# Performance work log

Hardware: AMD Instinct MI355X
Metric: run time of the kernel (lower is better)

Reference implementation:

```python
import jax, jax.numpy as jnp
import numpy as np

N, D, H, L, T, R = 50000, 128, 8, 2, 4, 8
E = 800000
HD = D // H  # head_size = 16
SQRT_D = float(np.sqrt(HD))


def typed_linear(x, types, W):
    # x: (n, Din), types: (n,), W: (T, Din, Dout)  -- per-type dense projection
    out = jnp.zeros((x.shape[0], W.shape[-1]), x.dtype)
    for t in range(W.shape[0]):
        out = out + jnp.where((types == t)[:, None], x @ W[t], 0.0)
    return out


def rel_typed(x, etype, W):
    # x: (E, H, d), etype: (E,), W: (H, R, d, d) -- per-head, per-edge-type linear
    out = jnp.zeros_like(x)
    for r in range(W.shape[1]):
        out = out + jnp.where((etype == r)[:, None, None], jnp.einsum('ehd,hdo->eho', x, W[:, r]), 0.0)
    return out


def edge_softmax(a, dst, n):
    # softmax over incoming edges per destination node, per head. a: (E, H)
    amax = jax.ops.segment_max(a, dst, num_segments=n)
    amax = jnp.where(jnp.isfinite(amax), amax, 0.0)
    ex = jnp.exp(a - amax[dst])
    s = jax.ops.segment_sum(ex, dst, num_segments=n)
    return ex / (s[dst] + 1e-9)


def layer_norm(x, g, b, eps=1e-5):
    mu = x.mean(-1, keepdims=True)
    var = ((x - mu) ** 2).mean(-1, keepdims=True)
    return (x - mu) * jax.lax.rsqrt(var + eps) * g + b


def hgt_conv(x, ntype, etype, src, dst, Wk, Wq, Wv, Wa, ratt, rmsg, rpri, skip):
    n = x.shape[0]
    k = typed_linear(x, ntype, Wk).reshape(n, H, HD)
    q = typed_linear(x, ntype, Wq).reshape(n, H, HD)
    v = typed_linear(x, ntype, Wv).reshape(n, H, HD)
    kw = rel_typed(k[src], etype, ratt)               # (E, H, d)
    pri = rpri[:, etype].T                            # (E, H)
    a = (kw * q[dst]).sum(-1) * pri / SQRT_D          # (E, H)
    m = rel_typed(v[src], etype, rmsg)                # (E, H, d)
    att = edge_softmax(a, dst, n)                     # (E, H)
    h = jax.ops.segment_sum(m * att[..., None], dst, num_segments=n)
    h = h.reshape(n, D)
    h = typed_linear(h, ntype, Wa)                    # dropout off (eval)
    alpha = jax.nn.sigmoid(skip[ntype])[:, None]
    return h * alpha + x * (1.0 - alpha)


def setup_inputs() -> dict:
    key = jax.random.key(0)
    ks = jax.random.split(key, 12)
    g_lin = float(np.sqrt(2.0 / (D + D)))   # xavier-ish scale for D x D
    g_rel = float(np.sqrt(2.0 / (HD + HD)))
    g_emb = float(np.sqrt(2.0 / (N + D)))
    return {
        'embed': jax.random.normal(ks[0], (T, N, D), jnp.float32) * g_emb,
        'Wk': jax.random.normal(ks[1], (L, T, D, D), jnp.float32) * g_lin,
        'Wq': jax.random.normal(ks[2], (L, T, D, D), jnp.float32) * g_lin,
        'Wv': jax.random.normal(ks[3], (L, T, D, D), jnp.float32) * g_lin,
        'Wa': jax.random.normal(ks[4], (L, T, D, D), jnp.float32) * g_lin,
        'rel_att': jax.random.normal(ks[5], (L, H, R, HD, HD), jnp.float32) * g_rel,
        'rel_msg': jax.random.normal(ks[6], (L, H, R, HD, HD), jnp.float32) * g_rel,
        'rel_pri': jnp.ones((L, H, R), jnp.float32),
        'skip': jnp.ones((L, T), jnp.float32),
        'ln_g': jnp.ones((L, D), jnp.float32),
        'ln_b': jnp.zeros((L, D), jnp.float32),
        'src': jax.random.randint(ks[7], (E,), 0, N, jnp.int32),
        'dst': jax.random.randint(ks[8], (E,), 0, N, jnp.int32),
        'ntype': jax.random.randint(ks[9], (N,), 0, T, jnp.int32),
        'etype': jax.random.randint(ks[10], (E,), 0, R, jnp.int32),
    }


def reference(embed, Wk, Wq, Wv, Wa, rel_att, rel_msg, rel_pri, skip, ln_g, ln_b, src, dst, ntype, etype):
    # masked per-type embedding init: node gets row <rank-within-its-type> of its type table
    onehot = jax.nn.one_hot(ntype, T, dtype=jnp.int32)
    rank = jnp.take_along_axis(jnp.cumsum(onehot, axis=0), ntype[:, None], axis=1)[:, 0] - 1
    h = embed[ntype, rank]                            # (N, D)
    for l in range(L):
        h_prev = h
        hc = hgt_conv(h, ntype, etype, src, dst,
                      Wk[l], Wq[l], Wv[l], Wa[l],
                      rel_att[l], rel_msg[l], rel_pri[l], skip[l])
        h = layer_norm(hc, ln_g[l], ln_b[l]) + h_prev
    return h
```

## Files before the change

kernel.cpp:

```cpp
#include <hip/hip_runtime.h>
#include <math.h>

#define N_NODES 50000
#define DIM     128
#define NHEAD   8
#define HDIM    16
#define NLAYER  2
#define NTYPE   4
#define NREL    8
#define NEDGE   800000
#define RB      256
#define GN      8
#define MT      32
#define NK      (N_NODES * NREL)

typedef __attribute__((ext_vector_type(8))) short bf16x8;
typedef __attribute__((ext_vector_type(4))) float f32x4;

__device__ __forceinline__ float blo(unsigned w) { return __uint_as_float(w << 16); }
__device__ __forceinline__ float bhi(unsigned w) { return __uint_as_float(w & 0xFFFF0000u); }
__device__ __forceinline__ unsigned short f2bf(float f) {
    unsigned b = __float_as_uint(f);
    b += 0x7FFFu + ((b >> 16) & 1u);
    return (unsigned short)(b >> 16);
}
__device__ __forceinline__ bf16x8 pack8(float4 x0, float4 x1) {
    bf16x8 r;
    r[0] = (short)f2bf(x0.x); r[1] = (short)f2bf(x0.y);
    r[2] = (short)f2bf(x0.z); r[3] = (short)f2bf(x0.w);
    r[4] = (short)f2bf(x1.x); r[5] = (short)f2bf(x1.y);
    r[6] = (short)f2bf(x1.z); r[7] = (short)f2bf(x1.w);
    return r;
}


__global__ void k_hist(const int* __restrict__ ntype, int* __restrict__ hist, int n) {
    __shared__ int cnt[NTYPE];
    if (threadIdx.x < NTYPE) cnt[threadIdx.x] = 0;
    __syncthreads();
    int i = blockIdx.x * RB + threadIdx.x;
    if (i < n) atomicAdd(&cnt[ntype[i]], 1);
    __syncthreads();
    if (threadIdx.x < NTYPE) hist[blockIdx.x * NTYPE + threadIdx.x] = cnt[threadIdx.x];
}

__global__ void k_prefix(const int* __restrict__ hist, int* __restrict__ off, int nb) {
    int t = threadIdx.x;
    if (t >= NTYPE) return;
    int acc = 0;
    for (int b = 0; b < nb; b++) { off[b * NTYPE + t] = acc; acc += hist[b * NTYPE + t]; }
}

__global__ void k_rank(const int* __restrict__ ntype, const int* __restrict__ off,
                       int* __restrict__ rank, int n) {
    __shared__ int ty[RB];
    int i = blockIdx.x * RB + threadIdx.x;
    int t = (i < n) ? ntype[i] : -1;
    ty[threadIdx.x] = t;
    __syncthreads();
    if (i < n) {
        int c = 0;
        for (int j = 0; j < (int)threadIdx.x; j++) c += (ty[j] == t);
        rank[i] = off[blockIdx.x * NTYPE + t] + c;
    }
}

__global__ void k_embed(const float* __restrict__ embed, const int* __restrict__ ntype,
                        const int* __restrict__ rank, float* __restrict__ h) {
    int i = blockIdx.x;
    int t = ntype[i], r = rank[i];
    h[(size_t)i * DIM + threadIdx.x] = embed[((size_t)t * N_NODES + r) * DIM + threadIdx.x];
}

__global__ void k_typeoff(const int* __restrict__ hist, const int* __restrict__ boff,
                          int nb, int* __restrict__ typeoff) {
    if (threadIdx.x == 0 && blockIdx.x == 0) {
        int acc = 0;
        for (int t = 0; t < NTYPE; t++) {
            typeoff[t] = acc;
            acc += boff[(nb - 1) * NTYPE + t] + hist[(nb - 1) * NTYPE + t];
        }
    }
}

__global__ void k_perm(const int* __restrict__ ntype, const int* __restrict__ rank,
                       const int* __restrict__ typeoff, int* __restrict__ perm, int n) {
    int i = blockIdx.x * 256 + threadIdx.x;
    if (i < n) perm[typeoff[ntype[i]] + rank[i]] = i;
}


__global__ void k_deg2(const int* __restrict__ dst, const int* __restrict__ etype,
                       int* __restrict__ deg) {
    int e = blockIdx.x * 256 + threadIdx.x;
    if (e < NEDGE) atomicAdd(&deg[dst[e] * NREL + etype[e]], 1);
}

__global__ void k_scan1(const int* __restrict__ deg, int* __restrict__ rs,
                        int* __restrict__ bsum, int n) {
    __shared__ int sh[256];
    int i = blockIdx.x * 256 + threadIdx.x;
    int v = (i < n) ? deg[i] : 0;
    sh[threadIdx.x] = v;
    __syncthreads();
    for (int off = 1; off < 256; off <<= 1) {
        int x = (threadIdx.x >= off) ? sh[threadIdx.x - off] : 0;
        __syncthreads();
        sh[threadIdx.x] += x;
        __syncthreads();
    }
    if (i < n) rs[i] = sh[threadIdx.x] - v;
    if (threadIdx.x == 255) bsum[blockIdx.x] = sh[255];
}

__global__ void k_scan2b(int* __restrict__ bsum, int nb) {
    __shared__ int sh[256];
    __shared__ int carry;
    if (threadIdx.x == 0) carry = 0;
    __syncthreads();
    for (int base = 0; base < nb; base += 256) {
        int i = base + threadIdx.x;
        int v = (i < nb) ? bsum[i] : 0;
        sh[threadIdx.x] = v;
        __syncthreads();
        for (int off = 1; off < 256; off <<= 1) {
            int x = (threadIdx.x >= off) ? sh[threadIdx.x - off] : 0;
            __syncthreads();
            sh[threadIdx.x] += x;
            __syncthreads();
        }
        if (i < nb) bsum[i] = sh[threadIdx.x] - v + carry;
        __syncthreads();
        if (threadIdx.x == 0) carry += sh[255];
        __syncthreads();
    }
}

__global__ void k_scan3(int* __restrict__ rs, const int* __restrict__ bsum, int n) {
    int i = blockIdx.x * 256 + threadIdx.x;
    if (i < n) rs[i] += bsum[blockIdx.x];
    if (i == 0) rs[n] = NEDGE;
}

__global__ void k_scatter2(const int* __restrict__ src, const int* __restrict__ dst,
                           const int* __restrict__ etype, const int* __restrict__ rs,
                           int* __restrict__ cur, int* __restrict__ epk) {
    int e = blockIdx.x * 256 + threadIdx.x;
    if (e < NEDGE) {
        int et = etype[e];
        int key = dst[e] * NREL + et;
        int p = atomicAdd(&cur[key], 1);
        epk[rs[key] + p] = src[e] | (et << 24);
    }
}


__global__ void k_rmsgT(const float* __restrict__ rmsg, float* __restrict__ rmsgT) {
    int b = blockIdx.x;
    int d = threadIdx.x >> 4, o = threadIdx.x & 15;
    rmsgT[b * 256 + o * 16 + d] = rmsg[b * 256 + d * 16 + o];
}

__global__ void k_rattB(const float* __restrict__ ratt, unsigned short* __restrict__ rattB) {
    int i = blockIdx.x * 256 + threadIdx.x;
    rattB[i] = f2bf(ratt[i]);
}

__global__ void k_packW(const float* __restrict__ W, unsigned short* __restrict__ WB) {
    int t = blockIdx.x;
    const float* w = W + (size_t)t * 16384;
    unsigned short* ob = WB + (size_t)t * 16384;
    for (int idx = threadIdx.x; idx < 16384; idx += 256) {
        int ct = idx >> 11, kc = (idx >> 9) & 3, l = (idx >> 3) & 63, j = idx & 7;
        int k = kc * 32 + ((l >> 4) << 3) + j;
        int c = ct * 16 + (l & 15);
        ob[idx] = f2bf(w[k * 128 + c]);
    }
}


__global__ __launch_bounds__(256) void k_qkv_mfma(
        const float* __restrict__ h, const int* __restrict__ perm, const int* __restrict__ ntype,
        const float* __restrict__ Wk, const float* __restrict__ Wq, const float* __restrict__ Wv,
        const unsigned short* __restrict__ WkB, const unsigned short* __restrict__ WqB,
        const unsigned short* __restrict__ WvB, const float* __restrict__ rmsgT,
        unsigned short* __restrict__ kb, float* __restrict__ qout,
        unsigned short* __restrict__ vt, int n) {
    int tid = threadIdx.x;
    int base = blockIdx.x * MT;
    __shared__ int nodes_s[MT];
    __shared__ int types_s[MT];
    __shared__ float vs[MT][132];

    if (tid < MT) {
        int idx = base + tid;
        int nd = (idx < n) ? perm[idx] : -1;
        nodes_s[tid] = nd;
        types_s[tid] = (nd >= 0) ? ntype[nd] : -1;
    }
    __syncthreads();
    bool same = (nodes_s[MT - 1] >= 0) && (types_s[0] == types_s[MT - 1]);

    if (same) {
        int l = tid & 63, w = tid >> 6;
        int t = types_s[0];
        const unsigned short* wbk = WkB + (size_t)t * 16384;
        const unsigned short* wbq = WqB + (size_t)t * 16384;
        const unsigned short* wbv = WvB + (size_t)t * 16384;
        f32x4 acc[3][2][2];
        #pragma unroll
        for (int m = 0; m < 3; m++)
            #pragma unroll
            for (int a = 0; a < 2; a++)
                #pragma unroll
                for (int b = 0; b < 2; b++) {
                    acc[m][a][b][0] = 0.f; acc[m][a][b][1] = 0.f;
                    acc[m][a][b][2] = 0.f; acc[m][a][b][3] = 0.f;
                }
        #pragma unroll 1
        for (int kc = 0; kc < 4; kc++) {
            int koff = kc * 32 + ((l >> 4) << 3);
            int r0 = l & 15;
            const float4* p0 = (const float4*)(h + (size_t)nodes_s[r0] * DIM + koff);
            bf16x8 a0 = pack8(p0[0], p0[1]);
            const float4* p1 = (const float4*)(h + (size_t)nodes_s[16 + r0] * DIM + koff);
            bf16x8 a1 = pack8(p1[0], p1[1]);
            #pragma unroll
            for (int cti = 0; cti < 2; cti++) {
                int boff = ((w * 2 + cti) * 4 + kc) * 512 + l * 8;
                bf16x8 bk = *(const bf16x8*)(wbk + boff);
                acc[0][0][cti] = __builtin_amdgcn_mfma_f32_16x16x32_bf16(a0, bk, acc[0][0][cti], 0, 0, 0);
                acc[0][1][cti] = __builtin_amdgcn_mfma_f32_16x16x32_bf16(a1, bk, acc[0][1][cti], 0, 0, 0);
                bf16x8 bq = *(const bf16x8*)(wbq + boff);
                acc[1][0][cti] = __builtin_amdgcn_mfma_f32_16x16x32_bf16(a0, bq, acc[1][0][cti], 0, 0, 0);
                acc[1][1][cti] = __builtin_amdgcn_mfma_f32_16x16x32_bf16(a1, bq, acc[1][1][cti], 0, 0, 0);
                bf16x8 bv = *(const bf16x8*)(wbv + boff);
                acc[2][0][cti] = __builtin_amdgcn_mfma_f32_16x16x32_bf16(a0, bv, acc[2][0][cti], 0, 0, 0);
                acc[2][1][cti] = __builtin_amdgcn_mfma_f32_16x16x32_bf16(a1, bv, acc[2][1][cti], 0, 0, 0);
            }
        }
        #pragma unroll
        for (int mt = 0; mt < 2; mt++)
            #pragma unroll
            for (int cti = 0; cti < 2; cti++) {
                int col = w * 32 + cti * 16 + (l & 15);
                #pragma unroll
                for (int r = 0; r < 4; r++) {
                    int row = mt * 16 + ((l >> 4) << 2) + r;
                    size_t p = (size_t)nodes_s[row] * DIM + col;
                    kb[p] = f2bf(acc[0][mt][cti][r]);
                    qout[p] = acc[1][mt][cti][r];
                    vs[row][col] = acc[2][mt][cti][r];
                }
            }
    } else {
        int o = tid & 127, half = tid >> 7;
        for (int nn = half; nn < MT; nn += 2) {
            int nd = nodes_s[nn];
            if (nd < 0) continue;
            int t = types_s[nn];
            const float* wk = Wk + (size_t)t * 16384;
            const float* wq = Wq + (size_t)t * 16384;
            const float* wv = Wv + (size_t)t * 16384;
            float ak = 0.f, aq = 0.f, av = 0.f;
            for (int d = 0; d < DIM; d++) {
                float xv = h[(size_t)nd * DIM + d];
                ak = fmaf(xv, wk[d * DIM + o], ak);
                aq = fmaf(xv, wq[d * DIM + o], aq);
                av = fmaf(xv, wv[d * DIM + o], av);
            }
            size_t p = (size_t)nd * DIM + o;
            kb[p] = f2bf(ak); qout[p] = aq;
            vs[nn][o] = av;
        }
    }
    __syncthreads();
    {
        int o = tid & 127, half = tid >> 7;
        int hh = o >> 4, oo = o & 15;
        #pragma unroll 1
        for (int et = 0; et < NREL; et++) {
            const float4* w4 = (const float4*)(rmsgT + ((size_t)(hh * NREL + et) * HDIM + oo) * HDIM);
            float4 w0 = w4[0], w1 = w4[1], w2 = w4[2], w3 = w4[3];
            for (int i = 0; i < 16; i++) {
                int nn = half * 16 + i;
                int nd = nodes_s[nn];
                if (nd < 0) continue;
                const float4* v4 = (const float4*)&vs[nn][hh * HDIM];
                float4 v0 = v4[0], v1 = v4[1], v2 = v4[2], v3 = v4[3];
                float a2 = v0.x*w0.x + v0.y*w0.y + v0.z*w0.z + v0.w*w0.w
                         + v1.x*w1.x + v1.y*w1.y + v1.z*w1.z + v1.w*w1.w
                         + v2.x*w2.x + v2.y*w2.y + v2.z*w2.z + v2.w*w2.w
                         + v3.x*w3.x + v3.y*w3.y + v3.z*w3.z + v3.w*w3.w;
                vt[((size_t)nd * NREL + et) * DIM + o] = f2bf(a2);
            }
        }
    }
}


__global__ __launch_bounds__(128) void k_fused10(
        const unsigned short* __restrict__ kb, const float* __restrict__ qbuf,
        const unsigned short* __restrict__ vt,
        const int* __restrict__ rs2, const int* __restrict__ epk,
        const unsigned short* __restrict__ rattB, const float* __restrict__ rpri,
        float* __restrict__ agg) {
    int node = blockIdx.x;
    int tid = threadIdx.x;
    int hh = tid >> 4, oo = tid & 15;
    int wv = tid >> 6;
    int hl = hh & 3;

    __shared__ float q_s[DIM];
    __shared__ float u_s[NREL][NHEAD * HDIM + 4];
    __shared__ float a_sw[2][4][HDIM + 1];
    __shared__ int   es_sw[2][HDIM];

    int e0 = rs2[node * NREL];
    int e1 = rs2[node * NREL + NREL];
    if (e0 == e1) { agg[(size_t)node * DIM + tid] = 0.f; return; }

    q_s[tid] = qbuf[(size_t)node * DIM + tid];
    {
        const float4* q4 = (const float4*)&q_s[hh * HDIM];
        float4 q0 = q4[0], q1 = q4[1], q2 = q4[2], q3 = q4[3];
        #pragma unroll
        for (int et = 0; et < NREL; et++) {
            const uint4* wB = (const uint4*)(rattB + ((size_t)(hh * NREL + et) * HDIM + oo) * HDIM);
            uint4 wa = wB[0], wb = wB[1];
            float s = blo(wa.x)*q0.x + bhi(wa.x)*q0.y + blo(wa.y)*q0.z + bhi(wa.y)*q0.w
                    + blo(wa.z)*q1.x + bhi(wa.z)*q1.y + blo(wa.w)*q1.z + bhi(wa.w)*q1.w
                    + blo(wb.x)*q2.x + bhi(wb.x)*q2.y + blo(wb.y)*q2.z + bhi(wb.y)*q2.w
                    + blo(wb.z)*q3.x + bhi(wb.z)*q3.y + blo(wb.w)*q3.z + bhi(wb.w)*q3.w;
            u_s[et][tid] = s * rpri[hh * NREL + et] * 0.25f;
        }
    }

    float m_h = -1e30f, s_h = 0.f, out = 0.f;

    for (int w0e = e0; w0e < e1; w0e += HDIM) {
        int cnt = min(HDIM, e1 - w0e);
        float a = -1e30f;
        int pk = 0;
        if (oo < cnt) {
            pk = epk[w0e + oo];
            int sv = pk & 0x00FFFFFF;
            int et = ((unsigned)pk) >> 24;
            const uint4* kr = (const uint4*)(kb + (size_t)sv * DIM + hh * HDIM);
            uint4 ka = kr[0], kc = kr[1];
            const float4* u4 = (const float4*)&u_s[et][hh * HDIM];
            float4 u0 = u4[0], u1 = u4[1], u2 = u4[2], u3 = u4[3];
            a = blo(ka.x)*u0.x + bhi(ka.x)*u0.y + blo(ka.y)*u0.z + bhi(ka.y)*u0.w
              + blo(ka.z)*u1.x + bhi(ka.z)*u1.y + blo(ka.w)*u1.z + bhi(ka.w)*u1.w
              + blo(kc.x)*u2.x + bhi(kc.x)*u2.y + blo(kc.y)*u2.z + bhi(kc.y)*u2.w
              + blo(kc.z)*u3.x + bhi(kc.z)*u3.y + blo(kc.w)*u3.z + bhi(kc.w)*u3.w;
        }
        if (hl == 0) es_sw[wv][oo] = pk;
        float cmax = a;
        cmax = fmaxf(cmax, __shfl_xor(cmax, 1));
        cmax = fmaxf(cmax, __shfl_xor(cmax, 2));
        cmax = fmaxf(cmax, __shfl_xor(cmax, 4));
        cmax = fmaxf(cmax, __shfl_xor(cmax, 8));
        float m_t = (cmax > m_h + 12.f) ? cmax : m_h;
        float r = __expf(m_h - m_t);
        s_h *= r; out *= r; m_h = m_t;
        float p = (oo < cnt) ? __expf(a - m_h) : 0.f;
        float ps = p;
        ps += __shfl_xor(ps, 1);
        ps += __shfl_xor(ps, 2);
        ps += __shfl_xor(ps, 4);
        ps += __shfl_xor(ps, 8);
        s_h += ps;
        a_sw[wv][hl][oo] = p;
        for (int c = 0; c < cnt; c++) {
            float pc = a_sw[wv][hl][c];
            int pkc = es_sw[wv][c];
            int sv = pkc & 0x00FFFFFF;
            int et = ((unsigned)pkc) >> 24;
            unsigned short uv = vt[((size_t)sv * NREL + et) * DIM + tid];
            out = fmaf(pc, __uint_as_float((unsigned)uv << 16), out);
        }
    }

    agg[(size_t)node * DIM + tid] = out / (s_h + 1e-9f);
}


__global__ __launch_bounds__(128) void k_out_g(
        const float* __restrict__ agg, float* __restrict__ h,
        const int* __restrict__ perm, const int* __restrict__ ntype,
        const float* __restrict__ Wa, const float* __restrict__ skip,
        const float* __restrict__ ln_g, const float* __restrict__ ln_b, int n) {
    int o = threadIdx.x;
    int base = blockIdx.x * GN;
    __shared__ float xs[GN][DIM];
    __shared__ float hcs[GN][DIM + 1];
    __shared__ int nodes[GN];
    __shared__ int types[GN];
    __shared__ float mu_s[GN], rs_s[GN];
    if (o < GN) {
        int idx = base + o;
        int nd = (idx < n) ? perm[idx] : -1;
        nodes[o] = nd;
        types[o] = (nd >= 0) ? ntype[nd] : -1;
    }
    __syncthreads();
    #pragma unroll
    for (int nn = 0; nn < GN; nn++)
        if (nodes[nn] >= 0) xs[nn][o] = agg[(size_t)nodes[nn] * DIM + o];
    __syncthreads();
    bool same = (nodes[GN - 1] >= 0) && (types[0] == types[GN - 1]);
    if (same) {
        int t = types[0];
        const float* w = Wa + (size_t)t * DIM * DIM;
        float acc[GN];
        #pragma unroll
        for (int nn = 0; nn < GN; nn++) acc[nn] = 0.f;
        for (int d = 0; d < DIM; d++) {
            float wv = w[d * DIM + o];
            #pragma unroll
            for (int nn = 0; nn < GN; nn++) acc[nn] = fmaf(xs[nn][d], wv, acc[nn]);
        }
        float alpha = 1.f / (1.f + __expf(-skip[t]));
        #pragma unroll
        for (int nn = 0; nn < GN; nn++) {
            float hp = h[(size_t)nodes[nn] * DIM + o];
            hcs[nn][o] = acc[nn] * alpha + hp * (1.f - alpha);
        }
    } else {
        #pragma unroll 1
        for (int nn = 0; nn < GN; nn++) {
            if (nodes[nn] < 0) continue;
            int t = types[nn];
            const float* w = Wa + (size_t)t * DIM * DIM;
            float a0 = 0.f;
            for (int d = 0; d < DIM; d++) a0 = fmaf(xs[nn][d], w[d * DIM + o], a0);
            float alpha = 1.f / (1.f + __expf(-skip[t]));
            float hp = h[(size_t)nodes[nn] * DIM + o];
            hcs[nn][o] = a0 * alpha + hp * (1.f - alpha);
        }
    }
    __syncthreads();
    {
        int g = o >> 4, j = o & 15;
        if (nodes[g] >= 0) {
            float s = 0.f;
            for (int d = j; d < DIM; d += 16) s += hcs[g][d];
            #pragma unroll
            for (int m = 1; m < 16; m <<= 1) s += __shfl_xor(s, m);
            float mu = s * (1.f / DIM);
            float v = 0.f;
            for (int d = j; d < DIM; d += 16) { float dv = hcs[g][d] - mu; v = fmaf(dv, dv, v); }
            #pragma unroll
            for (int m = 1; m < 16; m <<= 1) v += __shfl_xor(v, m);
            if (j == 0) { mu_s[g] = mu; rs_s[g] = rsqrtf(v * (1.f / DIM) + 1e-5f); }
        }
    }
    __syncthreads();
    float g_o = ln_g[o], b_o = ln_b[o];
    #pragma unroll
    for (int nn = 0; nn < GN; nn++) {
        if (nodes[nn] >= 0) {
            float hp = h[(size_t)nodes[nn] * DIM + o];
            h[(size_t)nodes[nn] * DIM + o] = (hcs[nn][o] - mu_s[nn]) * rs_s[nn] * g_o + b_o + hp;
        }
    }
}


extern "C" void kernel_launch(void* const* d_in, const int* in_sizes, int n_in,
                              void* d_out, int out_size, void* d_ws, size_t ws_size,
                              hipStream_t stream) {
    const float* embed = (const float*)d_in[0];
    const float* Wk    = (const float*)d_in[1];
    const float* Wq    = (const float*)d_in[2];
    const float* Wv    = (const float*)d_in[3];
    const float* Wa    = (const float*)d_in[4];
    const float* ratt  = (const float*)d_in[5];
    const float* rmsg  = (const float*)d_in[6];
    const float* rpri  = (const float*)d_in[7];
    const float* skip  = (const float*)d_in[8];
    const float* ln_g  = (const float*)d_in[9];
    const float* ln_b  = (const float*)d_in[10];
    const int*   src   = (const int*)d_in[11];
    const int*   dst   = (const int*)d_in[12];
    const int*   ntype = (const int*)d_in[13];
    const int*   etype = (const int*)d_in[14];

    float* h = (float*)d_out;

    const size_t ND = (size_t)N_NODES * DIM;
    const int nb = (N_NODES + RB - 1) / RB;
    unsigned short* kb = (unsigned short*)d_ws;
    float* qbuf = (float*)(kb + ND);
    int* rs2  = (int*)(qbuf + ND);
    int* deg2 = rs2 + (NK + 1);
    int* cur2 = deg2 + NK;
    int* epk  = cur2 + NK;
    int* bsum = epk + NEDGE;
    int* rank = bsum + 2048;
    int* hist = rank + N_NODES;
    int* boff = hist + nb * NTYPE;
    int* typeoff = boff + nb * NTYPE;
    int* perm = typeoff + NTYPE;
    float* rmsgT = (float*)(perm + N_NODES);
    unsigned short* rattB = (unsigned short*)(rmsgT + (size_t)NLAYER * NHEAD * NREL * 256);
    unsigned short* vt = rattB + (size_t)NLAYER * NHEAD * NREL * 256;
    unsigned short* wpk = vt + (size_t)N_NODES * NREL * DIM;
    float* agg = qbuf;

    const int EB = (NEDGE + 255) / 256;
    const int nb2 = (NK + 255) / 256;

    k_hist<<<nb, RB, 0, stream>>>(ntype, hist, N_NODES);
    k_prefix<<<1, 64, 0, stream>>>(hist, boff, nb);
    k_rank<<<nb, RB, 0, stream>>>(ntype, boff, rank, N_NODES);
    k_embed<<<N_NODES, DIM, 0, stream>>>(embed, ntype, rank, h);
    k_typeoff<<<1, 64, 0, stream>>>(hist, boff, nb, typeoff);
    k_perm<<<nb, 256, 0, stream>>>(ntype, rank, typeoff, perm, N_NODES);

    hipMemsetAsync(deg2, 0, (size_t)NK * sizeof(int), stream);
    hipMemsetAsync(cur2, 0, (size_t)NK * sizeof(int), stream);
    k_deg2<<<EB, 256, 0, stream>>>(dst, etype, deg2);
    k_scan1<<<nb2, 256, 0, stream>>>(deg2, rs2, bsum, NK);
    k_scan2b<<<1, 256, 0, stream>>>(bsum, nb2);
    k_scan3<<<nb2, 256, 0, stream>>>(rs2, bsum, NK);
    k_scatter2<<<EB, 256, 0, stream>>>(src, dst, etype, rs2, cur2, epk);

    k_rmsgT<<<NLAYER * NHEAD * NREL, 256, 0, stream>>>(rmsg, rmsgT);
    k_rattB<<<NLAYER * NHEAD * NREL, 256, 0, stream>>>(ratt, rattB);
    for (int l = 0; l < NLAYER; l++) {
        k_packW<<<NTYPE, 256, 0, stream>>>(Wk + (size_t)l * NTYPE * 16384,
                                           wpk + ((size_t)l * 3 + 0) * NTYPE * 16384);
        k_packW<<<NTYPE, 256, 0, stream>>>(Wq + (size_t)l * NTYPE * 16384,
                                           wpk + ((size_t)l * 3 + 1) * NTYPE * 16384);
        k_packW<<<NTYPE, 256, 0, stream>>>(Wv + (size_t)l * NTYPE * 16384,
                                           wpk + ((size_t)l * 3 + 2) * NTYPE * 16384);
    }

    const int NGB = N_NODES / GN;
    const int NMB = (N_NODES + MT - 1) / MT;

    for (int l = 0; l < NLAYER; l++) {
        const float* Wk_l = Wk + (size_t)l * NTYPE * DIM * DIM;
        const float* Wq_l = Wq + (size_t)l * NTYPE * DIM * DIM;
        const float* Wv_l = Wv + (size_t)l * NTYPE * DIM * DIM;
        const float* Wa_l = Wa + (size_t)l * NTYPE * DIM * DIM;
        const unsigned short* wkB_l = wpk + ((size_t)l * 3 + 0) * NTYPE * 16384;
        const unsigned short* wqB_l = wpk + ((size_t)l * 3 + 1) * NTYPE * 16384;
        const unsigned short* wvB_l = wpk + ((size_t)l * 3 + 2) * NTYPE * 16384;
        const unsigned short* rattB_l = rattB + (size_t)l * NHEAD * NREL * 256;
        const float* rmsgT_l = rmsgT + (size_t)l * NHEAD * NREL * 256;
        const float* rpri_l = rpri + (size_t)l * NHEAD * NREL;
        const float* skip_l = skip + (size_t)l * NTYPE;
        const float* g_l = ln_g + (size_t)l * DIM;
        const float* b_l = ln_b + (size_t)l * DIM;

        k_qkv_mfma<<<NMB, 256, 0, stream>>>(h, perm, ntype, Wk_l, Wq_l, Wv_l,
                                            wkB_l, wqB_l, wvB_l, rmsgT_l,
                                            kb, qbuf, vt, N_NODES);
        k_fused10<<<N_NODES, 128, 0, stream>>>(kb, qbuf, vt, rs2, epk,
                                               rattB_l, rpri_l, agg);
        k_out_g<<<NGB, 128, 0, stream>>>(agg, h, perm, ntype, Wa_l, skip_l, g_l, b_l, N_NODES);
    }
}
```

Before: 808.1 us.

## Store K/Q/V and aggregates in type-sorted order via inverse permutation

Intermediate buffers (kb, qbuf, vt, agg) are now indexed by type-sorted position instead of node id. An inverse permutation rewrites edge source indices once, at CSR build time. The QKV kernel writes contiguously, the output kernel reads agg contiguously, and the edge kernel maps each block to a node through perm. The six weight-packing launches are merged into one. The aim is to turn scattered writes into coalesced ones, at the cost of an extra permutation array and an indirect node lookup in the attention kernel.

Result: faster. 755.6 us (-6.5%).

```diff
diff --git a/kernel.cpp b/kernel.cpp
--- a/kernel.cpp
+++ b/kernel.cpp
@@ -84,9 +84,14 @@
 }
 
 __global__ void k_perm(const int* __restrict__ ntype, const int* __restrict__ rank,
-                       const int* __restrict__ typeoff, int* __restrict__ perm, int n) {
+                       const int* __restrict__ typeoff, int* __restrict__ perm,
+                       int* __restrict__ iperm, int n) {
     int i = blockIdx.x * 256 + threadIdx.x;
-    if (i < n) perm[typeoff[ntype[i]] + rank[i]] = i;
+    if (i < n) {
+        int p = typeoff[ntype[i]] + rank[i];
+        perm[p] = i;
+        iperm[i] = p;
+    }
 }
 
 
@@ -143,17 +148,23 @@
 }
 
 __global__ void k_scatter2(const int* __restrict__ src, const int* __restrict__ dst,
-                           const int* __restrict__ etype, const int* __restrict__ rs,
+                           const int* __restrict__ etype, const int* __restrict__ iperm,
+                           const int* __restrict__ rs,
                            int* __restrict__ cur, int* __restrict__ epk) {
     int e = blockIdx.x * 256 + threadIdx.x;
     if (e < NEDGE) {
         int et = etype[e];
         int key = dst[e] * NREL + et;
         int p = atomicAdd(&cur[key], 1);
-        epk[rs[key] + p] = src[e] | (et << 24);
-    }
-}
-
+        epk[rs[key] + p] = iperm[src[e]] | (et << 24);
+    }
+}
+
+
+__global__ void k_rattB(const float* __restrict__ ratt, unsigned short* __restrict__ rattB) {
+    int i = blockIdx.x * 256 + threadIdx.x;
+    rattB[i] = f2bf(ratt[i]);
+}
 
 __global__ void k_rmsgT(const float* __restrict__ rmsg, float* __restrict__ rmsgT) {
     int b = blockIdx.x;
@@ -161,20 +172,19 @@
     rmsgT[b * 256 + o * 16 + d] = rmsg[b * 256 + d * 16 + o];
 }
 
-__global__ void k_rattB(const float* __restrict__ ratt, unsigned short* __restrict__ rattB) {
-    int i = blockIdx.x * 256 + threadIdx.x;
-    rattB[i] = f2bf(ratt[i]);
-}
-
-__global__ void k_packW(const float* __restrict__ W, unsigned short* __restrict__ WB) {
-    int t = blockIdx.x;
-    const float* w = W + (size_t)t * 16384;
-    unsigned short* ob = WB + (size_t)t * 16384;
+__global__ void k_packW_all(const float* __restrict__ Wk, const float* __restrict__ Wq,
+                            const float* __restrict__ Wv, unsigned short* __restrict__ wpk) {
+    int bid = blockIdx.x;
+    int t = bid & 3;
+    int m = (bid >> 2) % 3;
+    int l = bid / 12;
+    const float* W = (m == 0 ? Wk : (m == 1 ? Wq : Wv)) + ((size_t)l * NTYPE + t) * 16384;
+    unsigned short* ob = wpk + (size_t)bid * 16384;
     for (int idx = threadIdx.x; idx < 16384; idx += 256) {
-        int ct = idx >> 11, kc = (idx >> 9) & 3, l = (idx >> 3) & 63, j = idx & 7;
-        int k = kc * 32 + ((l >> 4) << 3) + j;
-        int c = ct * 16 + (l & 15);
-        ob[idx] = f2bf(w[k * 128 + c]);
+        int ct = idx >> 11, kc = (idx >> 9) & 3, ln = (idx >> 3) & 63, j = idx & 7;
+        int k = kc * 32 + ((ln >> 4) << 3) + j;
+        int c = ct * 16 + (ln & 15);
+        ob[idx] = f2bf(W[k * 128 + c]);
     }
 }
 
@@ -200,9 +210,9 @@
     }
     __syncthreads();
     bool same = (nodes_s[MT - 1] >= 0) && (types_s[0] == types_s[MT - 1]);
+    int l = tid & 63, w = tid >> 6;
 
     if (same) {
-        int l = tid & 63, w = tid >> 6;
         int t = types_s[0];
         const unsigned short* wbk = WkB + (size_t)t * 16384;
         const unsigned short* wbq = WqB + (size_t)t * 16384;
@@ -247,7 +257,7 @@
                 #pragma unroll
                 for (int r = 0; r < 4; r++) {
                     int row = mt * 16 + ((l >> 4) << 2) + r;
-                    size_t p = (size_t)nodes_s[row] * DIM + col;
+                    size_t p = (size_t)(base + row) * DIM + col;
                     kb[p] = f2bf(acc[0][mt][cti][r]);
                     qout[p] = acc[1][mt][cti][r];
                     vs[row][col] = acc[2][mt][cti][r];
@@ -257,7 +267,7 @@
         int o = tid & 127, half = tid >> 7;
         for (int nn = half; nn < MT; nn += 2) {
             int nd = nodes_s[nn];
-            if (nd < 0) continue;
+            if (nd < 0) { vs[nn][o] = 0.f; continue; }
             int t = types_s[nn];
             const float* wk = Wk + (size_t)t * 16384;
             const float* wq = Wq + (size_t)t * 16384;
@@ -269,7 +279,7 @@
                 aq = fmaf(xv, wq[d * DIM + o], aq);
                 av = fmaf(xv, wv[d * DIM + o], av);
             }
-            size_t p = (size_t)nd * DIM + o;
+            size_t p = (size_t)(base + nn) * DIM + o;
             kb[p] = f2bf(ak); qout[p] = aq;
             vs[nn][o] = av;
         }
@@ -284,28 +294,29 @@
             float4 w0 = w4[0], w1 = w4[1], w2 = w4[2], w3 = w4[3];
             for (int i = 0; i < 16; i++) {
                 int nn = half * 16 + i;
-                int nd = nodes_s[nn];
-                if (nd < 0) continue;
+                if (base + nn >= n) continue;
                 const float4* v4 = (const float4*)&vs[nn][hh * HDIM];
                 float4 v0 = v4[0], v1 = v4[1], v2 = v4[2], v3 = v4[3];
                 float a2 = v0.x*w0.x + v0.y*w0.y + v0.z*w0.z + v0.w*w0.w
                          + v1.x*w1.x + v1.y*w1.y + v1.z*w1.z + v1.w*w1.w
                          + v2.x*w2.x + v2.y*w2.y + v2.z*w2.z + v2.w*w2.w
                          + v3.x*w3.x + v3.y*w3.y + v3.z*w3.z + v3.w*w3.w;
-                vt[((size_t)nd * NREL + et) * DIM + o] = f2bf(a2);
+                vt[((size_t)(base + nn) * NREL + et) * DIM + o] = f2bf(a2);
             }
         }
     }
 }
 
 
-__global__ __launch_bounds__(128) void k_fused10(
+__global__ __launch_bounds__(128) void k_fused11(
         const unsigned short* __restrict__ kb, const float* __restrict__ qbuf,
         const unsigned short* __restrict__ vt,
+        const int* __restrict__ perm,
         const int* __restrict__ rs2, const int* __restrict__ epk,
         const unsigned short* __restrict__ rattB, const float* __restrict__ rpri,
         float* __restrict__ agg) {
-    int node = blockIdx.x;
+    int b = blockIdx.x;
+    int node = perm[b];
     int tid = threadIdx.x;
     int hh = tid >> 4, oo = tid & 15;
     int wv = tid >> 6;
@@ -318,9 +329,9 @@
 
     int e0 = rs2[node * NREL];
     int e1 = rs2[node * NREL + NREL];
-    if (e0 == e1) { agg[(size_t)node * DIM + tid] = 0.f; return; }
-
-    q_s[tid] = qbuf[(size_t)node * DIM + tid];
+    if (e0 == e1) { agg[(size_t)b * DIM + tid] = 0.f; return; }
+
+    q_s[tid] = qbuf[(size_t)b * DIM + tid];
     {
         const float4* q4 = (const float4*)&q_s[hh * HDIM];
         float4 q0 = q4[0], q1 = q4[1], q2 = q4[2], q3 = q4[3];
@@ -382,7 +393,7 @@
         }
     }
 
-    agg[(size_t)node * DIM + tid] = out / (s_h + 1e-9f);
+    agg[(size_t)b * DIM + tid] = out / (s_h + 1e-9f);
 }
 
 
@@ -407,7 +418,7 @@
     __syncthreads();
     #pragma unroll
     for (int nn = 0; nn < GN; nn++)
-        if (nodes[nn] >= 0) xs[nn][o] = agg[(size_t)nodes[nn] * DIM + o];
+        if (nodes[nn] >= 0) xs[nn][o] = agg[(size_t)(base + nn) * DIM + o];
     __syncthreads();
     bool same = (nodes[GN - 1] >= 0) && (types[0] == types[GN - 1]);
     if (same) {
@@ -503,7 +514,8 @@
     int* boff = hist + nb * NTYPE;
     int* typeoff = boff + nb * NTYPE;
     int* perm = typeoff + NTYPE;
-    float* rmsgT = (float*)(perm + N_NODES);
+    int* iperm = perm + N_NODES;
+    float* rmsgT = (float*)(iperm + N_NODES);
     unsigned short* rattB = (unsigned short*)(rmsgT + (size_t)NLAYER * NHEAD * NREL * 256);
     unsigned short* vt = rattB + (size_t)NLAYER * NHEAD * NREL * 256;
     unsigned short* wpk = vt + (size_t)N_NODES * NREL * DIM;
@@ -517,7 +529,7 @@
     k_rank<<<nb, RB, 0, stream>>>(ntype, boff, rank, N_NODES);
     k_embed<<<N_NODES, DIM, 0, stream>>>(embed, ntype, rank, h);
     k_typeoff<<<1, 64, 0, stream>>>(hist, boff, nb, typeoff);
-    k_perm<<<nb, 256, 0, stream>>>(ntype, rank, typeoff, perm, N_NODES);
+    k_perm<<<nb, 256, 0, stream>>>(ntype, rank, typeoff, perm, iperm, N_NODES);
 
     hipMemsetAsync(deg2, 0, (size_t)NK * sizeof(int), stream);
     hipMemsetAsync(cur2, 0, (size_t)NK * sizeof(int), stream);
@@ -525,18 +537,11 @@
     k_scan1<<<nb2, 256, 0, stream>>>(deg2, rs2, bsum, NK);
     k_scan2b<<<1, 256, 0, stream>>>(bsum, nb2);
     k_scan3<<<nb2, 256, 0, stream>>>(rs2, bsum, NK);
-    k_scatter2<<<EB, 256, 0, stream>>>(src, dst, etype, rs2, cur2, epk);
-
+    k_scatter2<<<EB, 256, 0, stream>>>(src, dst, etype, iperm, rs2, cur2, epk);
+
+    k_rattB<<<NLAYER * NHEAD * NREL, 256, 0, stream>>>(ratt, rattB);
     k_rmsgT<<<NLAYER * NHEAD * NREL, 256, 0, stream>>>(rmsg, rmsgT);
-    k_rattB<<<NLAYER * NHEAD * NREL, 256, 0, stream>>>(ratt, rattB);
-    for (int l = 0; l < NLAYER; l++) {
-        k_packW<<<NTYPE, 256, 0, stream>>>(Wk + (size_t)l * NTYPE * 16384,
-                                           wpk + ((size_t)l * 3 + 0) * NTYPE * 16384);
-        k_packW<<<NTYPE, 256, 0, stream>>>(Wq + (size_t)l * NTYPE * 16384,
-                                           wpk + ((size_t)l * 3 + 1) * NTYPE * 16384);
-        k_packW<<<NTYPE, 256, 0, stream>>>(Wv + (size_t)l * NTYPE * 16384,
-                                           wpk + ((size_t)l * 3 + 2) * NTYPE * 16384);
-    }
+    k_packW_all<<<NLAYER * 3 * NTYPE, 256, 0, stream>>>(Wk, Wq, Wv, wpk);
 
     const int NGB = N_NODES / GN;
     const int NMB = (N_NODES + MT - 1) / MT;
@@ -559,7 +564,7 @@
         k_qkv_mfma<<<NMB, 256, 0, stream>>>(h, perm, ntype, Wk_l, Wq_l, Wv_l,
                                             wkB_l, wqB_l, wvB_l, rmsgT_l,
                                             kb, qbuf, vt, N_NODES);
-        k_fused10<<<N_NODES, 128, 0, stream>>>(kb, qbuf, vt, rs2, epk,
+        k_fused11<<<N_NODES, 128, 0, stream>>>(kb, qbuf, vt, perm, rs2, epk,
                                                rattB_l, rpri_l, agg);
         k_out_g<<<NGB, 128, 0, stream>>>(agg, h, perm, ntype, Wa_l, skip_l, g_l, b_l, N_NODES);
     }
```
